# Optimization experiments

Hardware: AMD Instinct MI355X
Metric: run time of the kernel (lower is better)

The kernel has to match this reference:

```python
import jax, jax.numpy as jnp
import numpy as np

P = 16; N_SIDE = 14; N_PATCH = 196
ENC_DIM = 1024; ENC_DEPTH = 2; ENC_HEADS = 16; ENC_DH = 64
DEC_DIM = 512; DEC_DEPTH = 1; DEC_HEADS = 8; DEC_DH = 64
NUM_MASKED = int(0.75 * N_PATCH)  # 147


def _ln(x, s, b):
    m = jnp.mean(x, axis=-1, keepdims=True)
    v = jnp.var(x, axis=-1, keepdims=True)
    return (x - m) * jax.lax.rsqrt(v + 1e-5) * s + b


def _mha(x, Wqkv, Wo, heads, dh):
    B, N, _ = x.shape
    q, k, v = jnp.split(x @ Wqkv, 3, axis=-1)
    rs = lambda t: t.reshape(B, N, heads, dh).transpose(0, 2, 1, 3)
    q, k, v = rs(q), rs(k), rs(v)
    scores = jnp.einsum('bhqd,bhkd->bhqk', q, k) / jnp.sqrt(jnp.float32(dh))
    att = jax.nn.softmax(scores, axis=-1)
    o = jnp.einsum('bhqk,bhkd->bhqd', att, v).transpose(0, 2, 1, 3).reshape(B, N, heads * dh)
    return o @ Wo


def _transformer(x, params, depth, heads, dh, lnfs, lnfb):
    (ln1s, ln1b, Wqkv, Wo, ln2s, ln2b, W1, b1, W2, b2) = params
    for i in range(depth):
        x = x + _mha(_ln(x, ln1s[i], ln1b[i]), Wqkv[i], Wo[i], heads, dh)
        h = jax.nn.gelu(_ln(x, ln2s[i], ln2b[i]) @ W1[i] + b1[i])
        x = x + h @ W2[i] + b2[i]
    return _ln(x, lnfs, lnfb)


def setup_inputs() -> dict:
    key = jax.random.key(0)
    ks = jax.random.split(key, 24)
    B = 64
    w = lambda k, s: (jax.random.normal(k, s, jnp.float32) * 0.02)
    E, IE = ENC_DIM, ENC_HEADS * ENC_DH
    D, ID = DEC_DIM, DEC_HEADS * DEC_DH
    d = {}
    d['images'] = jax.random.normal(ks[0], (B, 224, 224, 3), jnp.float32)
    d['rand'] = jax.random.uniform(ks[1], (B, N_PATCH), dtype=jnp.float32)
    d['patch_W'] = w(ks[2], (P * P * 3, E)); d['patch_b'] = jnp.zeros((E,), jnp.float32)
    d['pos_emb'] = w(ks[3], (N_PATCH, E))
    d['enc_ln1s'] = jnp.ones((ENC_DEPTH, E), jnp.float32); d['enc_ln1b'] = jnp.zeros((ENC_DEPTH, E), jnp.float32)
    d['enc_Wqkv'] = w(ks[4], (ENC_DEPTH, E, 3 * IE)); d['enc_Wo'] = w(ks[5], (ENC_DEPTH, IE, E))
    d['enc_ln2s'] = jnp.ones((ENC_DEPTH, E), jnp.float32); d['enc_ln2b'] = jnp.zeros((ENC_DEPTH, E), jnp.float32)
    d['enc_W1'] = w(ks[6], (ENC_DEPTH, E, 4 * E)); d['enc_b1'] = jnp.zeros((ENC_DEPTH, 4 * E), jnp.float32)
    d['enc_W2'] = w(ks[7], (ENC_DEPTH, 4 * E, E)); d['enc_b2'] = jnp.zeros((ENC_DEPTH, E), jnp.float32)
    d['enc_lnfs'] = jnp.ones((E,), jnp.float32); d['enc_lnfb'] = jnp.zeros((E,), jnp.float32)
    d['e2d_W'] = w(ks[8], (E, D)); d['e2d_b'] = jnp.zeros((D,), jnp.float32)
    d['mask_token'] = w(ks[9], (D,))
    d['dec_pos'] = w(ks[10], (N_PATCH, D))
    d['dec_ln1s'] = jnp.ones((DEC_DEPTH, D), jnp.float32); d['dec_ln1b'] = jnp.zeros((DEC_DEPTH, D), jnp.float32)
    d['dec_Wqkv'] = w(ks[11], (DEC_DEPTH, D, 3 * ID)); d['dec_Wo'] = w(ks[12], (DEC_DEPTH, ID, D))
    d['dec_ln2s'] = jnp.ones((DEC_DEPTH, D), jnp.float32); d['dec_ln2b'] = jnp.zeros((DEC_DEPTH, D), jnp.float32)
    d['dec_W1'] = w(ks[13], (DEC_DEPTH, D, 4 * D)); d['dec_b1'] = jnp.zeros((DEC_DEPTH, 4 * D), jnp.float32)
    d['dec_W2'] = w(ks[14], (DEC_DEPTH, 4 * D, D)); d['dec_b2'] = jnp.zeros((DEC_DEPTH, D), jnp.float32)
    d['dec_lnfs'] = jnp.ones((D,), jnp.float32); d['dec_lnfb'] = jnp.zeros((D,), jnp.float32)
    d['pix_W'] = w(ks[15], (D, E)); d['pix_b'] = jnp.zeros((E,), jnp.float32)  # pixel_dim == encoder_dim per source
    return d


def reference(images, rand, patch_W, patch_b, pos_emb,
              enc_ln1s, enc_ln1b, enc_Wqkv, enc_Wo, enc_ln2s, enc_ln2b,
              enc_W1, enc_b1, enc_W2, enc_b2, enc_lnfs, enc_lnfb,
              e2d_W, e2d_b, mask_token, dec_pos,
              dec_ln1s, dec_ln1b, dec_Wqkv, dec_Wo, dec_ln2s, dec_ln2b,
              dec_W1, dec_b1, dec_W2, dec_b2, dec_lnfs, dec_lnfb,
              pix_W, pix_b):
    B = images.shape[0]
    # patch embed: [B,224,224,3] -> [B,196,768] -> [B,196,1024]
    x = images.reshape(B, N_SIDE, P, N_SIDE, P, 3).transpose(0, 1, 3, 2, 4, 5).reshape(B, N_PATCH, P * P * 3)
    patches = x @ patch_W + patch_b
    tokens = patches + pos_emb
    # random masking via argsort of uniform noise
    order = jnp.argsort(rand, axis=-1)
    m_idx = order[:, :NUM_MASKED]        # [B,147]
    u_idx = order[:, NUM_MASKED:]        # [B,49]
    unmasked = jnp.take_along_axis(tokens, u_idx[:, :, None], axis=1)
    enc_params = (enc_ln1s, enc_ln1b, enc_Wqkv, enc_Wo, enc_ln2s, enc_ln2b, enc_W1, enc_b1, enc_W2, enc_b2)
    encoded = _transformer(unmasked, enc_params, ENC_DEPTH, ENC_HEADS, ENC_DH, enc_lnfs, enc_lnfb)
    dec_tok = encoded @ e2d_W + e2d_b + dec_pos[u_idx]
    mask_toks = mask_token + dec_pos[m_idx]
    bidx = jnp.arange(B)[:, None]
    all_tok = jnp.zeros((B, N_PATCH, DEC_DIM), dec_tok.dtype)
    all_tok = all_tok.at[bidx, u_idx].set(dec_tok)
    all_tok = all_tok.at[bidx, m_idx].set(mask_toks)
    dec_params = (dec_ln1s, dec_ln1b, dec_Wqkv, dec_Wo, dec_ln2s, dec_ln2b, dec_W1, dec_b1, dec_W2, dec_b2)
    decoded = _transformer(all_tok, dec_params, DEC_DEPTH, DEC_HEADS, DEC_DH, dec_lnfs, dec_lnfb)
    pred = jnp.take_along_axis(decoded, m_idx[:, :, None], axis=1) @ pix_W + pix_b
    target = jnp.take_along_axis(patches, m_idx[:, :, None], axis=1)
    return jnp.mean((pred - target) ** 2)
```

## Files before the change

### kernel.cpp

```cpp
#include <hip/hip_runtime.h>

typedef __attribute__((ext_vector_type(8))) __bf16 bf16x8;
typedef __attribute__((ext_vector_type(4))) float f32x4;

#define OFF_PATCH 0ull
#define OFF_X     25690112ull
#define OFF_LN    51380224ull
#define OFF_QKV   64225280ull
#define OFF_HID   103022592ull
#define OFF_WP    154402816ull
#define OFF_ORD   214695936ull
#define OFF_PART  214746112ull

#define WP_PATCH   0ull
#define WP_ENC_QKV 786432ull
#define WP_ENC_WO  7077888ull
#define WP_ENC_W1  9175040ull
#define WP_ENC_W2  17563648ull
#define WP_E2D     25952256ull
#define WP_DEC_QKV 26476544ull
#define WP_DEC_WO  27262976ull
#define WP_DEC_W1  27525120ull
#define WP_DEC_W2  28573696ull
#define WP_PIX     29622272ull

#define OM_BF16 0
#define OM_F32  1
#define OM_ACC  2
#define OM_GELU 3

__device__ __forceinline__ float b2f(unsigned short u) {
    return __uint_as_float(((unsigned int)u) << 16);
}
__device__ __forceinline__ unsigned short f2b(float f) {
    unsigned int x = __float_as_uint(f);
    x += 0x7fffu + ((x >> 16) & 1u);
    return (unsigned short)(x >> 16);
}
__device__ __forceinline__ float gelu_f(float x) {
    float u2 = 1.5957691216057308f * x * (1.f + 0.044715f * x * x);
    return x / (1.f + __expf(-u2));
}
__device__ __forceinline__ void gload16(const void* g, void* l) {
    __builtin_amdgcn_global_load_lds((const __attribute__((address_space(1))) void*)g,
                                     (__attribute__((address_space(3))) void*)l, 16, 0, 0);
}

__global__ __launch_bounds__(256) void pack_w(const float* __restrict__ in,
                                              unsigned short* __restrict__ out, int K, int N) {
    __shared__ float tile[32][33];
    int kt = blockIdx.y * 32, nt = blockIdx.x * 32;
    int tx = threadIdx.x & 31, ty = threadIdx.x >> 5;
#pragma unroll
    for (int i = 0; i < 32; i += 8) tile[ty + i][tx] = in[(size_t)(kt + ty + i) * N + nt + tx];
    __syncthreads();
#pragma unroll
    for (int i = 0; i < 32; i += 8)
        out[(size_t)(nt + ty + i) * K + kt + tx] = f2b(tile[tx][ty + i]);
}

__global__ __launch_bounds__(256) void patchify_kernel(const float* __restrict__ img,
                                                       unsigned short* __restrict__ Xp) {
    const long long total = 12544ll * 768;
    for (long long e = (long long)blockIdx.x * 256 + threadIdx.x; e < total;
         e += (long long)gridDim.x * 256) {
        int row = (int)(e / 768), k = (int)(e % 768);
        int b = row / 196, pi = row % 196;
        int py = pi / 14, px = pi % 14;
        int r = k / 48, rem = k % 48;
        int c = rem / 3, ch = rem % 3;
        long long src = (((long long)(b * 224 + py * 16 + r)) * 224 + (px * 16 + c)) * 3 + ch;
        Xp[e] = f2b(img[src]);
    }
}

template <int BM, int OM, bool ATOMIC>
__global__ __launch_bounds__((BM / 32) * 64) void gemm3(const unsigned short* __restrict__ A,
                                                        const unsigned short* __restrict__ Bt,
                                                        void* __restrict__ Cv,
                                                        const float* __restrict__ bias,
                                                        int M, int N, int K, int Kc) {
    constexpr int WAVES = BM / 32;
    constexpr int BRW = 128 / WAVES;
    constexpr int NIB = BRW / 8;
    __shared__ __align__(16) unsigned short S[BM * 64 + 128 * 64];
    const int tid = threadIdx.x, wave = tid >> 6, lane = tid & 63;
    int nwg = gridDim.x * gridDim.y;
    int orig = blockIdx.y * gridDim.x + blockIdx.x;
    int q = nwg >> 3, r8 = nwg & 7, xcd = orig & 7, off = orig >> 3;
    int wg = (xcd < r8 ? xcd * (q + 1) : r8 * (q + 1) + (xcd - r8) * q) + off;
    const int brow = (wg / gridDim.x) * BM, bcol = (wg % gridDim.x) * 128;
    const int kBeg = blockIdx.z * Kc;
    const int fr = lane & 15, fq = lane >> 4;
    const int wr = (wave >> 1) * 64, wc = (wave & 1) * 64;
    const int lr = lane >> 3;
    const int sca = ((lane & 7) ^ lr) * 8;
    const unsigned short* Agp[4];
#pragma unroll
    for (int i = 0; i < 4; ++i) {
        int r = brow + wave * 32 + i * 8 + lr;
        if (r > M - 1) r = M - 1;
        Agp[i] = A + (size_t)r * K + kBeg + sca;
    }
    const unsigned short* Bgp[NIB];
#pragma unroll
    for (int i = 0; i < NIB; ++i) {
        int r = bcol + wave * BRW + i * 8 + lr;
        Bgp[i] = Bt + (size_t)r * K + kBeg + sca;
    }

    f32x4 acc[4][4];
#pragma unroll
    for (int m = 0; m < 4; ++m)
#pragma unroll
        for (int n = 0; n < 4; ++n) acc[m][n] = (f32x4){0.f, 0.f, 0.f, 0.f};

    const char* lds = (const char*)S;
    const int sw = (fr & 7) << 4;
    const int a0 = (wr + fr) * 128 + ((fq * 16) ^ sw);
    const int b0 = BM * 128 + (wc + fr) * 128 + ((fq * 16) ^ sw);

    const int nt = Kc >> 6;
    for (int t = 0; t < nt; ++t) {
        __syncthreads();
        const int k0 = t << 6;
#pragma unroll
        for (int i = 0; i < 4; ++i)
            gload16(Agp[i] + k0, S + (wave * 32 + i * 8) * 64);
#pragma unroll
        for (int i = 0; i < NIB; ++i)
            gload16(Bgp[i] + k0, S + BM * 64 + (wave * BRW + i * 8) * 64);
        __syncthreads();
        __builtin_amdgcn_s_setprio(1);
#pragma unroll
        for (int kk = 0; kk < 2; ++kk) {
            const int kx = kk * 64;
            bf16x8 af[4], bf[4];
#pragma unroll
            for (int m = 0; m < 4; ++m)
                af[m] = *(const bf16x8*)(lds + ((a0 ^ kx) + m * 2048));
#pragma unroll
            for (int n = 0; n < 4; ++n)
                bf[n] = *(const bf16x8*)(lds + ((b0 ^ kx) + n * 2048));
#pragma unroll
            for (int m = 0; m < 4; ++m)
#pragma unroll
                for (int n = 0; n < 4; ++n)
                    acc[m][n] = __builtin_amdgcn_mfma_f32_16x16x32_bf16(af[m], bf[n],
                                                                       acc[m][n], 0, 0, 0);
        }
        __builtin_amdgcn_s_setprio(0);
    }

    const bool addBias = (bias != nullptr) && (kBeg == 0);
#pragma unroll
    for (int m = 0; m < 4; ++m) {
        int rb = brow + wr + m * 16 + fq * 4;
#pragma unroll
        for (int r = 0; r < 4; ++r) {
            int row = rb + r;
            if (row < M) {
#pragma unroll
                for (int n = 0; n < 4; ++n) {
                    int col = bcol + wc + n * 16 + fr;
                    float v = acc[m][n][r];
                    if (addBias) v += bias[col];
                    size_t o = (size_t)row * N + col;
                    if constexpr (ATOMIC) atomicAdd((float*)Cv + o, v);
                    else if constexpr (OM == OM_BF16) ((unsigned short*)Cv)[o] = f2b(v);
                    else if constexpr (OM == OM_F32) ((float*)Cv)[o] = v;
                    else if constexpr (OM == OM_ACC) ((float*)Cv)[o] += v;
                    else ((unsigned short*)Cv)[o] = f2b(gelu_f(v));
                }
            }
        }
    }
}

template <int N, int H, int NW>
__global__ __launch_bounds__(NW * 64) void attn_mfma(const unsigned short* __restrict__ qkv,
                                                     unsigned short* __restrict__ out) {
    constexpr int Npad = ((N + 31) / 32) * 32;
    constexpr int NT = Npad / 16;
    constexpr int KS = Npad / 32;
    constexpr int PS = Npad + 8;
    constexpr int SQ = 3 * H * 64, SO = H * 64;
    __shared__ __align__(16) unsigned short Kl[Npad * 64];
    __shared__ __align__(16) unsigned short Vt[64 * PS];
    __shared__ __align__(16) unsigned short Pl[NW * 16 * PS];
    const int b = blockIdx.x / H, h = blockIdx.x % H;
    const unsigned short* base = qkv + (size_t)b * N * SQ;
    const int qoff = h * 64, koff = (H + h) * 64, voff = (2 * H + h) * 64;
    const int tid = threadIdx.x, wave = tid >> 6, lane = tid & 63;
    const int fr = lane & 15, fq = lane >> 4;

    for (int idx = tid; idx < Npad * 8; idx += NW * 64) {
        int row = idx >> 3, ch = idx & 7;
        uint4 v = {0u, 0u, 0u, 0u};
        if (row < N) v = *(const uint4*)(base + (size_t)row * SQ + koff + ch * 8);
        *(uint4*)((char*)Kl + row * 128 + ((ch * 16) ^ ((row & 7) << 4))) = v;
    }
    for (int idx = tid; idx < Npad * 32; idx += NW * 64) {
        int key = idx >> 5, d2 = (idx & 31) * 2;
        unsigned int v = 0;
        if (key < N) v = *(const unsigned int*)(base + (size_t)key * SQ + voff + d2);
        Vt[d2 * PS + key] = (unsigned short)(v & 0xffffu);
        Vt[(d2 + 1) * PS + key] = (unsigned short)(v >> 16);
    }
    __syncthreads();

    unsigned short* pw = Pl + wave * 16 * PS;
    for (int qt = wave; qt < NT; qt += NW) {
        const int q0 = qt * 16;
        int qr = q0 + fr;
        if (qr > N - 1) qr = N - 1;
        const unsigned short* qp = base + (size_t)qr * SQ + qoff + fq * 8;
        bf16x8 aq0 = *(const bf16x8*)qp;
        bf16x8 aq1 = *(const bf16x8*)(qp + 32);
        f32x4 sa[NT];
#pragma unroll
        for (int ct = 0; ct < NT; ++ct) sa[ct] = (f32x4){0.f, 0.f, 0.f, 0.f};
#pragma unroll
        for (int ct = 0; ct < NT; ++ct) {
            const char* kb = (const char*)Kl + (ct * 16 + fr) * 128;
            bf16x8 kf0 = *(const bf16x8*)(kb + ((fq * 16) ^ ((fr & 7) << 4)));
            bf16x8 kf1 = *(const bf16x8*)(kb + ((64 + fq * 16) ^ ((fr & 7) << 4)));
            sa[ct] = __builtin_amdgcn_mfma_f32_16x16x32_bf16(aq0, kf0, sa[ct], 0, 0, 0);
            sa[ct] = __builtin_amdgcn_mfma_f32_16x16x32_bf16(aq1, kf1, sa[ct], 0, 0, 0);
        }
        float mrow[4] = {-3e38f, -3e38f, -3e38f, -3e38f};
#pragma unroll
        for (int ct = 0; ct < NT; ++ct) {
            bool ok = (ct * 16 + fr) < N;
#pragma unroll
            for (int r = 0; r < 4; ++r) {
                float s = ok ? sa[ct][r] * 0.125f : -3e38f;
                sa[ct][r] = s;
                mrow[r] = fmaxf(mrow[r], s);
            }
        }
#pragma unroll
        for (int off = 1; off <= 8; off <<= 1)
#pragma unroll
            for (int r = 0; r < 4; ++r) mrow[r] = fmaxf(mrow[r], __shfl_xor(mrow[r], off));
        float ssum[4] = {0.f, 0.f, 0.f, 0.f};
#pragma unroll
        for (int ct = 0; ct < NT; ++ct)
#pragma unroll
            for (int r = 0; r < 4; ++r) {
                float p = __expf(sa[ct][r] - mrow[r]);
                sa[ct][r] = p;
                ssum[r] += p;
            }
#pragma unroll
        for (int off = 1; off <= 8; off <<= 1)
#pragma unroll
            for (int r = 0; r < 4; ++r) ssum[r] += __shfl_xor(ssum[r], off);
#pragma unroll
        for (int ct = 0; ct < NT; ++ct)
#pragma unroll
            for (int r = 0; r < 4; ++r)
                pw[(fq * 4 + r) * PS + ct * 16 + fr] = f2b(sa[ct][r]);
        f32x4 oa[4];
#pragma unroll
        for (int vt = 0; vt < 4; ++vt) oa[vt] = (f32x4){0.f, 0.f, 0.f, 0.f};
#pragma unroll
        for (int ks = 0; ks < KS; ++ks) {
            bf16x8 pa = *(const bf16x8*)(pw + fr * PS + ks * 32 + fq * 8);
#pragma unroll
            for (int vt = 0; vt < 4; ++vt) {
                bf16x8 vf = *(const bf16x8*)(&Vt[(vt * 16 + fr) * PS + ks * 32 + fq * 8]);
                oa[vt] = __builtin_amdgcn_mfma_f32_16x16x32_bf16(pa, vf, oa[vt], 0, 0, 0);
            }
        }
        float inv[4];
#pragma unroll
        for (int r = 0; r < 4; ++r) inv[r] = 1.f / ssum[r];
#pragma unroll
        for (int vt = 0; vt < 4; ++vt)
#pragma unroll
            for (int r = 0; r < 4; ++r) {
                int q = q0 + fq * 4 + r;
                if (q < N)
                    out[((size_t)b * N + q) * SO + h * 64 + vt * 16 + fr] =
                        f2b(oa[vt][r] * inv[r]);
            }
    }
}

__global__ __launch_bounds__(256) void argsort_kernel(const float* __restrict__ rnd,
                                                      int* __restrict__ ord) {
    __shared__ float vals[196];
    int b = blockIdx.x, t = threadIdx.x;
    if (t < 196) vals[t] = rnd[b * 196 + t];
    __syncthreads();
    if (t < 196) {
        float v = vals[t];
        int rank = 0;
        for (int j = 0; j < 196; ++j) {
            float vj = vals[j];
            rank += (vj < v) || (vj == v && j < t);
        }
        ord[b * 196 + rank] = t;
    }
}

__global__ __launch_bounds__(256) void gather_unmasked(const unsigned short* __restrict__ patches,
                                                       const float* __restrict__ pos,
                                                       const int* __restrict__ ord,
                                                       float* __restrict__ xe) {
    int row = blockIdx.x;
    int b = row / 49, i = row % 49;
    int src = ord[b * 196 + 147 + i];
    const unsigned short* pr = patches + ((size_t)(b * 196 + src) << 10);
    const float* pe = pos + ((size_t)src << 10);
    float* o = xe + ((size_t)row << 10);
    int d = threadIdx.x * 4;
    ushort4 pv = *(const ushort4*)(pr + d);
    float4 p4 = *(const float4*)(pe + d);
    float4 r;
    r.x = b2f(pv.x) + p4.x; r.y = b2f(pv.y) + p4.y;
    r.z = b2f(pv.z) + p4.z; r.w = b2f(pv.w) + p4.w;
    *(float4*)(o + d) = r;
}

template <int L>
__global__ __launch_bounds__(256) void ln_kernel(const float* __restrict__ x,
                                                 unsigned short* __restrict__ y,
                                                 const float* __restrict__ sw,
                                                 const float* __restrict__ bw) {
    __shared__ float red[8];
    const int tid = threadIdx.x;
    const float* xr = x + (size_t)blockIdx.x * L;
    float sum = 0.f, sq = 0.f;
    for (int i = tid * 4; i < L; i += 1024) {
        float4 v = *(const float4*)(xr + i);
        sum += v.x + v.y + v.z + v.w;
        sq += v.x * v.x + v.y * v.y + v.z * v.z + v.w * v.w;
    }
    for (int off = 32; off; off >>= 1) {
        sum += __shfl_xor(sum, off);
        sq += __shfl_xor(sq, off);
    }
    int wave = tid >> 6, lane = tid & 63;
    if (lane == 0) { red[wave] = sum; red[4 + wave] = sq; }
    __syncthreads();
    float ts = red[0] + red[1] + red[2] + red[3];
    float tq = red[4] + red[5] + red[6] + red[7];
    float mean = ts / L;
    float inv = rsqrtf(tq / L - mean * mean + 1e-5f);
    unsigned short* yr = y + (size_t)blockIdx.x * L;
    for (int i = tid * 4; i < L; i += 1024) {
        float4 v = *(const float4*)(xr + i);
        float4 s4 = *(const float4*)(sw + i);
        float4 b4 = *(const float4*)(bw + i);
        ushort4 o;
        o.x = f2b((v.x - mean) * inv * s4.x + b4.x);
        o.y = f2b((v.y - mean) * inv * s4.y + b4.y);
        o.z = f2b((v.z - mean) * inv * s4.z + b4.z);
        o.w = f2b((v.w - mean) * inv * s4.w + b4.w);
        *(ushort4*)(yr + i) = o;
    }
}

__global__ __launch_bounds__(256) void scatter_tokens(const float* __restrict__ dec_tok,
                                                      const float* __restrict__ dec_pos,
                                                      const float* __restrict__ mask_tok,
                                                      const int* __restrict__ ord,
                                                      float* __restrict__ all_tok) {
    int e = blockIdx.x;
    int b = e / 196, i = e % 196;
    int idx = ord[e];
    float* o = all_tok + ((size_t)(b * 196 + idx)) * 512;
    const float* dp = dec_pos + (size_t)idx * 512;
    int d = threadIdx.x * 4;
    if (d < 512) {
        float4 dv = *(const float4*)(dp + d);
        float4 sv;
        if (i < 147) sv = *(const float4*)(mask_tok + d);
        else sv = *(const float4*)(dec_tok + ((size_t)(b * 49 + (i - 147))) * 512 + d);
        float4 r = {sv.x + dv.x, sv.y + dv.y, sv.z + dv.z, sv.w + dv.w};
        *(float4*)(o + d) = r;
    }
}

__global__ __launch_bounds__(256) void gather_masked(const unsigned short* __restrict__ x,
                                                     const int* __restrict__ ord,
                                                     unsigned short* __restrict__ gm) {
    int r = blockIdx.x;
    int b = r / 147, j = r % 147;
    int idx = ord[b * 196 + j];
    const unsigned short* src = x + ((size_t)(b * 196 + idx)) * 512;
    unsigned short* o = gm + (size_t)r * 512;
    int d = threadIdx.x * 4;
    if (d < 512) *(ushort4*)(o + d) = *(const ushort4*)(src + d);
}

__global__ __launch_bounds__(256) void loss_partial(const float* __restrict__ pred,
                                                    const unsigned short* __restrict__ patches,
                                                    const int* __restrict__ ord,
                                                    float* __restrict__ part) {
    __shared__ float red[8];
    float local = 0.f;
    const long long total = 9633792ll;
    for (long long e = (long long)blockIdx.x * 256 + threadIdx.x; e < total; e += 4096ll * 256) {
        int r = (int)(e >> 10), d = (int)(e & 1023);
        int b = r / 147, j = r % 147;
        int idx = ord[b * 196 + j];
        float t = b2f(patches[(((size_t)(b * 196 + idx)) << 10) + d]);
        float df = pred[e] - t;
        local += df * df;
    }
    for (int off = 32; off; off >>= 1) local += __shfl_xor(local, off);
    int wave = threadIdx.x >> 6, lane = threadIdx.x & 63;
    if (lane == 0) red[wave] = local;
    __syncthreads();
    if (threadIdx.x == 0) part[blockIdx.x] = red[0] + red[1] + red[2] + red[3];
}

__global__ __launch_bounds__(256) void loss_final(const float* __restrict__ part,
                                                  float* __restrict__ out) {
    __shared__ float red[8];
    float local = 0.f;
    for (int i = threadIdx.x; i < 4096; i += 256) local += part[i];
    for (int off = 32; off; off >>= 1) local += __shfl_xor(local, off);
    int wave = threadIdx.x >> 6, lane = threadIdx.x & 63;
    if (lane == 0) red[wave] = local;
    __syncthreads();
    if (threadIdx.x == 0) out[0] = (red[0] + red[1] + red[2] + red[3]) / 9633792.0f;
}

extern "C" void kernel_launch(void* const* d_in, const int* in_sizes, int n_in, void* d_out,
                              int out_size, void* d_ws, size_t ws_size, hipStream_t stream) {
    const float* images = (const float*)d_in[0];
    const float* rnd = (const float*)d_in[1];
    const float* patch_W = (const float*)d_in[2];
    const float* patch_b = (const float*)d_in[3];
    const float* pos_emb = (const float*)d_in[4];
    const float* enc_ln1s = (const float*)d_in[5];
    const float* enc_ln1b = (const float*)d_in[6];
    const float* enc_Wqkv = (const float*)d_in[7];
    const float* enc_Wo = (const float*)d_in[8];
    const float* enc_ln2s = (const float*)d_in[9];
    const float* enc_ln2b = (const float*)d_in[10];
    const float* enc_W1 = (const float*)d_in[11];
    const float* enc_b1 = (const float*)d_in[12];
    const float* enc_W2 = (const float*)d_in[13];
    const float* enc_b2 = (const float*)d_in[14];
    const float* enc_lnfs = (const float*)d_in[15];
    const float* enc_lnfb = (const float*)d_in[16];
    const float* e2d_W = (const float*)d_in[17];
    const float* e2d_b = (const float*)d_in[18];
    const float* mask_tok = (const float*)d_in[19];
    const float* dec_pos = (const float*)d_in[20];
    const float* dec_ln1s = (const float*)d_in[21];
    const float* dec_ln1b = (const float*)d_in[22];
    const float* dec_Wqkv = (const float*)d_in[23];
    const float* dec_Wo = (const float*)d_in[24];
    const float* dec_ln2s = (const float*)d_in[25];
    const float* dec_ln2b = (const float*)d_in[26];
    const float* dec_W1 = (const float*)d_in[27];
    const float* dec_b1 = (const float*)d_in[28];
    const float* dec_W2 = (const float*)d_in[29];
    const float* dec_b2 = (const float*)d_in[30];
    const float* dec_lnfs = (const float*)d_in[31];
    const float* dec_lnfb = (const float*)d_in[32];
    const float* pix_W = (const float*)d_in[33];
    const float* pix_b = (const float*)d_in[34];

    char* ws = (char*)d_ws;
    unsigned short* patches = (unsigned short*)(ws + OFF_PATCH);
    float* Rx = (float*)(ws + OFF_X);
    unsigned short* Rln = (unsigned short*)(ws + OFF_LN);
    unsigned short* RqkvB = (unsigned short*)(ws + OFF_QKV);
    float* RqkvF = (float*)(ws + OFF_QKV);
    unsigned short* Rhid = (unsigned short*)(ws + OFF_HID);
    unsigned short* wp = (unsigned short*)(ws + OFF_WP);
    int* ord = (int*)(ws + OFF_ORD);
    float* part = (float*)(ws + OFF_PART);
    float* out = (float*)d_out;

    auto PACK = [&](const float* src, size_t wpo, int K, int N) {
        pack_w<<<dim3(N / 32, K / 32), 256, 0, stream>>>(src, wp + wpo, K, N);
    };
    PACK(patch_W, WP_PATCH, 768, 1024);
    for (int l = 0; l < 2; ++l) {
        PACK(enc_Wqkv + (size_t)l * 1024 * 3072, WP_ENC_QKV + (size_t)l * 3145728, 1024, 3072);
        PACK(enc_Wo + (size_t)l * 1024 * 1024, WP_ENC_WO + (size_t)l * 1048576, 1024, 1024);
        PACK(enc_W1 + (size_t)l * 1024 * 4096, WP_ENC_W1 + (size_t)l * 4194304, 1024, 4096);
        PACK(enc_W2 + (size_t)l * 4096 * 1024, WP_ENC_W2 + (size_t)l * 4194304, 4096, 1024);
    }
    PACK(e2d_W, WP_E2D, 1024, 512);
    PACK(dec_Wqkv, WP_DEC_QKV, 512, 1536);
    PACK(dec_Wo, WP_DEC_WO, 512, 512);
    PACK(dec_W1, WP_DEC_W1, 512, 2048);
    PACK(dec_W2, WP_DEC_W2, 2048, 512);
    PACK(pix_W, WP_PIX, 512, 1024);

    auto GEMM = [&](int om, const unsigned short* A, size_t wpo, void* C, const float* bias,
                    int M, int N, int K, int S, bool small) {
        const unsigned short* Bt = wp + wpo;
        int Kc = K / S;
        if (!small) {
            dim3 g(N / 128, (M + 255) / 256, S);
            if (S > 1) gemm3<256, OM_ACC, true><<<g, 512, 0, stream>>>(A, Bt, C, bias, M, N, K, Kc);
            else if (om == OM_BF16) gemm3<256, OM_BF16, false><<<g, 512, 0, stream>>>(A, Bt, C, bias, M, N, K, Kc);
            else if (om == OM_F32) gemm3<256, OM_F32, false><<<g, 512, 0, stream>>>(A, Bt, C, bias, M, N, K, Kc);
            else if (om == OM_ACC) gemm3<256, OM_ACC, false><<<g, 512, 0, stream>>>(A, Bt, C, bias, M, N, K, Kc);
            else gemm3<256, OM_GELU, false><<<g, 512, 0, stream>>>(A, Bt, C, bias, M, N, K, Kc);
        } else {
            dim3 g(N / 128, (M + 127) / 128, S);
            if (S > 1) gemm3<128, OM_ACC, true><<<g, 256, 0, stream>>>(A, Bt, C, bias, M, N, K, Kc);
            else if (om == OM_BF16) gemm3<128, OM_BF16, false><<<g, 256, 0, stream>>>(A, Bt, C, bias, M, N, K, Kc);
            else if (om == OM_F32) gemm3<128, OM_F32, false><<<g, 256, 0, stream>>>(A, Bt, C, bias, M, N, K, Kc);
            else if (om == OM_ACC) gemm3<128, OM_ACC, false><<<g, 256, 0, stream>>>(A, Bt, C, bias, M, N, K, Kc);
            else gemm3<128, OM_GELU, false><<<g, 256, 0, stream>>>(A, Bt, C, bias, M, N, K, Kc);
        }
    };

    patchify_kernel<<<4096, 256, 0, stream>>>(images, Rhid);
    GEMM(OM_BF16, Rhid, WP_PATCH, patches, patch_b, 12544, 1024, 768, 1, false);
    argsort_kernel<<<64, 256, 0, stream>>>(rnd, ord);
    gather_unmasked<<<3136, 256, 0, stream>>>(patches, pos_emb, ord, Rx);

    for (int l = 0; l < 2; ++l) {
        ln_kernel<1024><<<3136, 256, 0, stream>>>(Rx, Rln, enc_ln1s + l * 1024,
                                                  enc_ln1b + l * 1024);
        GEMM(OM_BF16, Rln, WP_ENC_QKV + (size_t)l * 3145728, RqkvB, nullptr, 3136, 3072, 1024,
             1, false);
        attn_mfma<49, 16, 4><<<64 * 16, 256, 0, stream>>>(RqkvB, Rhid);
        GEMM(OM_ACC, Rhid, WP_ENC_WO + (size_t)l * 1048576, Rx, nullptr, 3136, 1024, 1024, 2,
             false);
        ln_kernel<1024><<<3136, 256, 0, stream>>>(Rx, Rln, enc_ln2s + l * 1024,
                                                  enc_ln2b + l * 1024);
        GEMM(OM_GELU, Rln, WP_ENC_W1 + (size_t)l * 4194304, Rhid, enc_b1 + l * 4096, 3136,
             4096, 1024, 1, false);
        GEMM(OM_ACC, Rhid, WP_ENC_W2 + (size_t)l * 4194304, Rx, enc_b2 + l * 1024, 3136, 1024,
             4096, 4, false);
    }
    ln_kernel<1024><<<3136, 256, 0, stream>>>(Rx, Rln, enc_lnfs, enc_lnfb);

    GEMM(OM_F32, Rln, WP_E2D, RqkvF, e2d_b, 3136, 512, 1024, 1, true);
    scatter_tokens<<<12544, 256, 0, stream>>>(RqkvF, dec_pos, mask_tok, ord, Rx);

    ln_kernel<512><<<12544, 256, 0, stream>>>(Rx, Rln, dec_ln1s, dec_ln1b);
    GEMM(OM_BF16, Rln, WP_DEC_QKV, RqkvB, nullptr, 12544, 1536, 512, 1, false);
    attn_mfma<196, 8, 8><<<64 * 8, 512, 0, stream>>>(RqkvB, Rhid);
    GEMM(OM_ACC, Rhid, WP_DEC_WO, Rx, nullptr, 12544, 512, 512, 1, false);
    ln_kernel<512><<<12544, 256, 0, stream>>>(Rx, Rln, dec_ln2s, dec_ln2b);
    GEMM(OM_GELU, Rln, WP_DEC_W1, Rhid, dec_b1, 12544, 2048, 512, 1, false);
    GEMM(OM_ACC, Rhid, WP_DEC_W2, Rx, dec_b2, 12544, 512, 2048, 2, false);
    ln_kernel<512><<<12544, 256, 0, stream>>>(Rx, Rln, dec_lnfs, dec_lnfb);

    gather_masked<<<9408, 256, 0, stream>>>(Rln, ord, Rhid);
    GEMM(OM_F32, Rhid, WP_PIX, RqkvF, pix_b, 9408, 1024, 512, 1, false);
    loss_partial<<<4096, 256, 0, stream>>>(RqkvF, patches, ord, part);
    loss_final<<<1, 256, 0, stream>>>(part, out);
}
```

Baseline: 852.1 us.

## Batch weight packing into one launch, fuse masked gather into GEMM, raise split-K

All fifteen per-weight transpose/convert launches are merged into a single pack_all kernel that finds its descriptor from a tile-start table. The masked-row gather before the pixel GEMM is folded into the GEMM's A-row address computation, which removes one kernel and an intermediate buffer round trip. Split-K for the encoder Wo GEMM goes from 2 to 4 and for the decoder Wo GEMM from 1 to 2, adding atomic accumulation traffic in exchange for more workgroups. The small-tile GEMM dispatch is also trimmed so it no longer handles OM_ACC or OM_GELU without split-K; no call in the shown code uses that path.

```diff
diff --git a/kernel.cpp b/kernel.cpp
--- a/kernel.cpp
+++ b/kernel.cpp
@@ -46,10 +46,23 @@
                                      (__attribute__((address_space(3))) void*)l, 16, 0, 0);
 }
 
-__global__ __launch_bounds__(256) void pack_w(const float* __restrict__ in,
-                                              unsigned short* __restrict__ out, int K, int N) {
+struct PackArgs {
+    const float* src[15];
+    unsigned long long dstOff[15];
+    int K[15], N[15];
+    int tileStart[16];
+};
+__global__ __launch_bounds__(256) void pack_all(PackArgs pa, unsigned short* __restrict__ wp) {
     __shared__ float tile[32][33];
-    int kt = blockIdx.y * 32, nt = blockIdx.x * 32;
+    int t = blockIdx.x;
+    int d = 0;
+    while (d < 14 && t >= pa.tileStart[d + 1]) ++d;
+    int local = t - pa.tileStart[d];
+    int K = pa.K[d], N = pa.N[d];
+    int ntn = N >> 5;
+    int kt = (local / ntn) << 5, nt = (local % ntn) << 5;
+    const float* in = pa.src[d];
+    unsigned short* out = wp + pa.dstOff[d];
     int tx = threadIdx.x & 31, ty = threadIdx.x >> 5;
 #pragma unroll
     for (int i = 0; i < 32; i += 8) tile[ty + i][tx] = in[(size_t)(kt + ty + i) * N + nt + tx];
@@ -74,11 +87,12 @@
     }
 }
 
-template <int BM, int OM, bool ATOMIC>
+template <int BM, int OM, bool ATOMIC, bool GATHER>
 __global__ __launch_bounds__((BM / 32) * 64) void gemm3(const unsigned short* __restrict__ A,
                                                         const unsigned short* __restrict__ Bt,
                                                         void* __restrict__ Cv,
                                                         const float* __restrict__ bias,
+                                                        const int* __restrict__ gord,
                                                         int M, int N, int K, int Kc) {
     constexpr int WAVES = BM / 32;
     constexpr int BRW = 128 / WAVES;
@@ -100,6 +114,10 @@
     for (int i = 0; i < 4; ++i) {
         int r = brow + wave * 32 + i * 8 + lr;
         if (r > M - 1) r = M - 1;
+        if constexpr (GATHER) {
+            int bb = r / 147, jj = r - bb * 147;
+            r = bb * 196 + gord[bb * 196 + jj];
+        }
         Agp[i] = A + (size_t)r * K + kBeg + sca;
     }
     const unsigned short* Bgp[NIB];
@@ -382,18 +400,6 @@
         float4 r = {sv.x + dv.x, sv.y + dv.y, sv.z + dv.z, sv.w + dv.w};
         *(float4*)(o + d) = r;
     }
-}
-
-__global__ __launch_bounds__(256) void gather_masked(const unsigned short* __restrict__ x,
-                                                     const int* __restrict__ ord,
-                                                     unsigned short* __restrict__ gm) {
-    int r = blockIdx.x;
-    int b = r / 147, j = r % 147;
-    int idx = ord[b * 196 + j];
-    const unsigned short* src = x + ((size_t)(b * 196 + idx)) * 512;
-    unsigned short* o = gm + (size_t)r * 512;
-    int d = threadIdx.x * 4;
-    if (d < 512) *(ushort4*)(o + d) = *(const ushort4*)(src + d);
 }
 
 __global__ __launch_bounds__(256) void loss_partial(const float* __restrict__ pred,
@@ -480,41 +486,47 @@
     float* part = (float*)(ws + OFF_PART);
     float* out = (float*)d_out;
 
-    auto PACK = [&](const float* src, size_t wpo, int K, int N) {
-        pack_w<<<dim3(N / 32, K / 32), 256, 0, stream>>>(src, wp + wpo, K, N);
+    PackArgs pa;
+    int nd = 0, tiles = 0;
+    auto ADDP = [&](const float* src, unsigned long long wpo, int K, int N) {
+        pa.src[nd] = src; pa.dstOff[nd] = wpo; pa.K[nd] = K; pa.N[nd] = N;
+        pa.tileStart[nd] = tiles;
+        tiles += (K >> 5) * (N >> 5);
+        ++nd;
     };
-    PACK(patch_W, WP_PATCH, 768, 1024);
+    ADDP(patch_W, WP_PATCH, 768, 1024);
     for (int l = 0; l < 2; ++l) {
-        PACK(enc_Wqkv + (size_t)l * 1024 * 3072, WP_ENC_QKV + (size_t)l * 3145728, 1024, 3072);
-        PACK(enc_Wo + (size_t)l * 1024 * 1024, WP_ENC_WO + (size_t)l * 1048576, 1024, 1024);
-        PACK(enc_W1 + (size_t)l * 1024 * 4096, WP_ENC_W1 + (size_t)l * 4194304, 1024, 4096);
-        PACK(enc_W2 + (size_t)l * 4096 * 1024, WP_ENC_W2 + (size_t)l * 4194304, 4096, 1024);
-    }
-    PACK(e2d_W, WP_E2D, 1024, 512);
-    PACK(dec_Wqkv, WP_DEC_QKV, 512, 1536);
-    PACK(dec_Wo, WP_DEC_WO, 512, 512);
-    PACK(dec_W1, WP_DEC_W1, 512, 2048);
-    PACK(dec_W2, WP_DEC_W2, 2048, 512);
-    PACK(pix_W, WP_PIX, 512, 1024);
+        ADDP(enc_Wqkv + (size_t)l * 1024 * 3072, WP_ENC_QKV + (size_t)l * 3145728, 1024, 3072);
+        ADDP(enc_Wo + (size_t)l * 1024 * 1024, WP_ENC_WO + (size_t)l * 1048576, 1024, 1024);
+        ADDP(enc_W1 + (size_t)l * 1024 * 4096, WP_ENC_W1 + (size_t)l * 4194304, 1024, 4096);
+        ADDP(enc_W2 + (size_t)l * 4096 * 1024, WP_ENC_W2 + (size_t)l * 4194304, 4096, 1024);
+    }
+    ADDP(e2d_W, WP_E2D, 1024, 512);
+    ADDP(dec_Wqkv, WP_DEC_QKV, 512, 1536);
+    ADDP(dec_Wo, WP_DEC_WO, 512, 512);
+    ADDP(dec_W1, WP_DEC_W1, 512, 2048);
+    ADDP(dec_W2, WP_DEC_W2, 2048, 512);
+    ADDP(pix_W, WP_PIX, 512, 1024);
+    pa.tileStart[nd] = tiles;
+    pack_all<<<tiles, 256, 0, stream>>>(pa, wp);
 
     auto GEMM = [&](int om, const unsigned short* A, size_t wpo, void* C, const float* bias,
-                    int M, int N, int K, int S, bool small) {
+                    int M, int N, int K, int S, bool small, const int* gord = nullptr) {
         const unsigned short* Bt = wp + wpo;
         int Kc = K / S;
         if (!small) {
             dim3 g(N / 128, (M + 255) / 256, S);
-            if (S > 1) gemm3<256, OM_ACC, true><<<g, 512, 0, stream>>>(A, Bt, C, bias, M, N, K, Kc);
-            else if (om == OM_BF16) gemm3<256, OM_BF16, false><<<g, 512, 0, stream>>>(A, Bt, C, bias, M, N, K, Kc);
-            else if (om == OM_F32) gemm3<256, OM_F32, false><<<g, 512, 0, stream>>>(A, Bt, C, bias, M, N, K, Kc);
-            else if (om == OM_ACC) gemm3<256, OM_ACC, false><<<g, 512, 0, stream>>>(A, Bt, C, bias, M, N, K, Kc);
-            else gemm3<256, OM_GELU, false><<<g, 512, 0, stream>>>(A, Bt, C, bias, M, N, K, Kc);
+            if (gord) gemm3<256, OM_F32, false, true><<<g, 512, 0, stream>>>(A, Bt, C, bias, gord, M, N, K, Kc);
+            else if (S > 1) gemm3<256, OM_ACC, true, false><<<g, 512, 0, stream>>>(A, Bt, C, bias, nullptr, M, N, K, Kc);
+            else if (om == OM_BF16) gemm3<256, OM_BF16, false, false><<<g, 512, 0, stream>>>(A, Bt, C, bias, nullptr, M, N, K, Kc);
+            else if (om == OM_F32) gemm3<256, OM_F32, false, false><<<g, 512, 0, stream>>>(A, Bt, C, bias, nullptr, M, N, K, Kc);
+            else if (om == OM_ACC) gemm3<256, OM_ACC, false, false><<<g, 512, 0, stream>>>(A, Bt, C, bias, nullptr, M, N, K, Kc);
+            else gemm3<256, OM_GELU, false, false><<<g, 512, 0, stream>>>(A, Bt, C, bias, nullptr, M, N, K, Kc);
         } else {
             dim3 g(N / 128, (M + 127) / 128, S);
-            if (S > 1) gemm3<128, OM_ACC, true><<<g, 256, 0, stream>>>(A, Bt, C, bias, M, N, K, Kc);
-            else if (om == OM_BF16) gemm3<128, OM_BF16, false><<<g, 256, 0, stream>>>(A, Bt, C, bias, M, N, K, Kc);
-            else if (om == OM_F32) gemm3<128, OM_F32, false><<<g, 256, 0, stream>>>(A, Bt, C, bias, M, N, K, Kc);
-            else if (om == OM_ACC) gemm3<128, OM_ACC, false><<<g, 256, 0, stream>>>(A, Bt, C, bias, M, N, K, Kc);
-            else gemm3<128, OM_GELU, false><<<g, 256, 0, stream>>>(A, Bt, C, bias, M, N, K, Kc);
+            if (S > 1) gemm3<128, OM_ACC, true, false><<<g, 256, 0, stream>>>(A, Bt, C, bias, nullptr, M, N, K, Kc);
+            else if (om == OM_F32) gemm3<128, OM_F32, false, false><<<g, 256, 0, stream>>>(A, Bt, C, bias, nullptr, M, N, K, Kc);
+            else gemm3<128, OM_BF16, false, false><<<g, 256, 0, stream>>>(A, Bt, C, bias, nullptr, M, N, K, Kc);
         }
     };
 
@@ -529,7 +541,7 @@
         GEMM(OM_BF16, Rln, WP_ENC_QKV + (size_t)l * 3145728, RqkvB, nullptr, 3136, 3072, 1024,
              1, false);
         attn_mfma<49, 16, 4><<<64 * 16, 256, 0, stream>>>(RqkvB, Rhid);
-        GEMM(OM_ACC, Rhid, WP_ENC_WO + (size_t)l * 1048576, Rx, nullptr, 3136, 1024, 1024, 2,
+        GEMM(OM_ACC, Rhid, WP_ENC_WO + (size_t)l * 1048576, Rx, nullptr, 3136, 1024, 1024, 4,
              false);
         ln_kernel<1024><<<3136, 256, 0, stream>>>(Rx, Rln, enc_ln2s + l * 1024,
                                                   enc_ln2b + l * 1024);
@@ -546,14 +558,13 @@
     ln_kernel<512><<<12544, 256, 0, stream>>>(Rx, Rln, dec_ln1s, dec_ln1b);
     GEMM(OM_BF16, Rln, WP_DEC_QKV, RqkvB, nullptr, 12544, 1536, 512, 1, false);
     attn_mfma<196, 8, 8><<<64 * 8, 512, 0, stream>>>(RqkvB, Rhid);
-    GEMM(OM_ACC, Rhid, WP_DEC_WO, Rx, nullptr, 12544, 512, 512, 1, false);
+    GEMM(OM_ACC, Rhid, WP_DEC_WO, Rx, nullptr, 12544, 512, 512, 2, false);
     ln_kernel<512><<<12544, 256, 0, stream>>>(Rx, Rln, dec_ln2s, dec_ln2b);
     GEMM(OM_GELU, Rln, WP_DEC_W1, Rhid, dec_b1, 12544, 2048, 512, 1, false);
     GEMM(OM_ACC, Rhid, WP_DEC_W2, Rx, dec_b2, 12544, 512, 2048, 2, false);
     ln_kernel<512><<<12544, 256, 0, stream>>>(Rx, Rln, dec_lnfs, dec_lnfb);
 
-    gather_masked<<<9408, 256, 0, stream>>>(Rln, ord, Rhid);
-    GEMM(OM_F32, Rhid, WP_PIX, RqkvF, pix_b, 9408, 1024, 512, 1, false);
+    GEMM(OM_F32, Rln, WP_PIX, RqkvF, pix_b, 9408, 1024, 512, 1, false, ord);
     loss_partial<<<4096, 256, 0, stream>>>(RqkvF, patches, ord, part);
     loss_final<<<1, 256, 0, stream>>>(part, out);
 }
```

New measurement: 863.8 us. About the same (+1.4%).
